# Performance work log

Hardware: AMD Instinct MI355X
Metric: run time of the kernel (lower is better)

Reference implementation:

```python
import jax, jax.numpy as jnp
import numpy as np

L, H, D, DH = 4, 16, 1024, 64   # n_layers, n_heads, d_model, head_dim
VOCAB = 32000
B, S = 2, 2048


def layer_norm(X):
    # Faithful to source: divides by variance (not std), no epsilon.
    mu = jnp.mean(X, axis=2, keepdims=True)
    var = jnp.mean((X - mu) ** 2, axis=2, keepdims=True)
    return (X - mu) / var


def setup_inputs() -> dict:
    key = jax.random.key(0)
    ks = jax.random.split(key, 12)
    s = 0.02
    X = jax.random.normal(ks[0], (B, S, D), dtype=jnp.float32)
    Wq = jax.random.normal(ks[1], (L, H, D, DH), dtype=jnp.float32) * s
    Wk = jax.random.normal(ks[2], (L, H, D, DH), dtype=jnp.float32) * s
    Wv = jax.random.normal(ks[3], (L, H, D, DH), dtype=jnp.float32) * s
    bq = jax.random.normal(ks[4], (L, H, DH), dtype=jnp.float32) * s
    bk = jax.random.normal(ks[5], (L, H, DH), dtype=jnp.float32) * s
    bv = jax.random.normal(ks[6], (L, H, DH), dtype=jnp.float32) * s
    Wffn = jax.random.normal(ks[7], (L, D, D), dtype=jnp.float32) * s
    bffn = jax.random.normal(ks[8], (L, D), dtype=jnp.float32) * s
    Wout = jax.random.normal(ks[9], (D, VOCAB), dtype=jnp.float32) * s
    bout = jax.random.normal(ks[10], (VOCAB,), dtype=jnp.float32) * s
    return {"X": X, "Wq": Wq, "Wk": Wk, "Wv": Wv, "bq": bq, "bk": bk,
            "bv": bv, "Wffn": Wffn, "bffn": bffn, "Wout": Wout, "bout": bout}


def reference(X, Wq, Wk, Wv, bq, bk, bv, Wffn, bffn, Wout, bout):
    sd = jnp.sqrt(jnp.float32(DH))
    for l in range(L):
        # All heads batched: [h, b, s, dh]
        Q = jnp.einsum('bsd,hde->hbse', X, Wq[l]) + bq[l][:, None, None, :]
        K = jnp.einsum('bsd,hde->hbse', X, Wk[l]) + bk[l][:, None, None, :]
        V = jnp.einsum('bsd,hde->hbse', X, Wv[l]) + bv[l][:, None, None, :]
        QK = jnp.einsum('hbse,hbte->hbst', Q, K) / sd
        # Faithful bug: softmax over full row, THEN tril mask (no renorm).
        A = jnp.tril(jax.nn.softmax(QK, axis=-1))
        Z = jnp.einsum('hbst,hbte->hbse', A, V)          # [h,b,s,dh]
        Z = jnp.transpose(Z, (1, 2, 0, 3)).reshape(X.shape[0], X.shape[1], D)
        X = layer_norm(X + Z)                            # note: W_o unused in source
        F = jax.nn.relu(X @ Wffn[l] + bffn[l])
        X = layer_norm(X + F)
    logits = X @ Wout + bout
    return jax.nn.softmax(logits, axis=2)[:, -1, :]
```

## Files before the change

### kernel.cpp

```cpp
#include <hip/hip_runtime.h>
#include <hip/hip_bf16.h>

#define NL 4
#define NH 16
#define DM 1024
#define DHD 64
#define NV 32000
#define NB 2
#define NS 2048
#define NM (NB * NS)

typedef __attribute__((ext_vector_type(8))) short v8s;
typedef __attribute__((ext_vector_type(4))) float v4f;

#define MFMA(a, b, c) __builtin_amdgcn_mfma_f32_16x16x32_bf16(a, b, c, 0, 0, 0)

__device__ __forceinline__ short f2bf(float x) {
    __hip_bfloat16 h = __float2bfloat16(x);
    return *reinterpret_cast<short*>(&h);
}
__device__ __forceinline__ float wave_sum(float v) {
    v += __shfl_xor(v, 32); v += __shfl_xor(v, 16); v += __shfl_xor(v, 8);
    v += __shfl_xor(v, 4);  v += __shfl_xor(v, 2);  v += __shfl_xor(v, 1);
    return v;
}
__device__ __forceinline__ float wave_max(float v) {
    v = fmaxf(v, __shfl_xor(v, 32)); v = fmaxf(v, __shfl_xor(v, 16));
    v = fmaxf(v, __shfl_xor(v, 8));  v = fmaxf(v, __shfl_xor(v, 4));
    v = fmaxf(v, __shfl_xor(v, 2));  v = fmaxf(v, __shfl_xor(v, 1));
    return v;
}

__global__ __launch_bounds__(256) void wqkv_transpose(
    const float* __restrict__ Wq, const float* __restrict__ Wk,
    const float* __restrict__ Wv, __hip_bfloat16* __restrict__ WT)
{
    __shared__ float T[64][68];
    const int t = threadIdx.x;
    const int k0 = blockIdx.x * 64;
    const int y = blockIdx.y;
    const int which = y >> 6, lh = y & 63;
    const float* W = (which == 0 ? Wq : which == 1 ? Wk : Wv)
                     + ((size_t)lh * DM + k0) * DHD;
#pragma unroll
    for (int i = 0; i < 4; ++i) {
        const int f = t + i * 256;
        const int kr = f >> 4, c = (f & 15) * 4;
        float4 w4 = *(const float4*)&W[(size_t)kr * DHD + c];
        T[kr][c + 0] = w4.x; T[kr][c + 1] = w4.y;
        T[kr][c + 2] = w4.z; T[kr][c + 3] = w4.w;
    }
    __syncthreads();
#pragma unroll
    for (int i = 0; i < 2; ++i) {
        const int f = t + i * 256;
        const int n = f >> 3, c = (f & 7) * 8;
        short tmp[8];
#pragma unroll
        for (int j = 0; j < 8; ++j) tmp[j] = f2bf(T[c + j][n]);
        *(float4*)&WT[(((size_t)y) * 64 + n) * DM + k0 + c] = *(float4*)tmp;
    }
}

__global__ __launch_bounds__(256) void wffn_transpose(
    const float* __restrict__ Wffn, __hip_bfloat16* __restrict__ WT)
{
    __shared__ float T[64][68];
    const int t = threadIdx.x;
    const int k0 = blockIdx.x * 64, n0 = blockIdx.y * 64, l = blockIdx.z;
    const float* W = Wffn + ((size_t)l * DM + k0) * DM + n0;
#pragma unroll
    for (int i = 0; i < 4; ++i) {
        const int f = t + i * 256;
        const int kr = f >> 4, c = (f & 15) * 4;
        float4 w4 = *(const float4*)&W[(size_t)kr * DM + c];
        T[kr][c + 0] = w4.x; T[kr][c + 1] = w4.y;
        T[kr][c + 2] = w4.z; T[kr][c + 3] = w4.w;
    }
    __syncthreads();
#pragma unroll
    for (int i = 0; i < 2; ++i) {
        const int f = t + i * 256;
        const int n = f >> 3, c = (f & 7) * 8;
        short tmp[8];
#pragma unroll
        for (int j = 0; j < 8; ++j) tmp[j] = f2bf(T[c + j][n]);
        *(float4*)&WT[((size_t)l * DM + n0 + n) * DM + k0 + c] = *(float4*)tmp;
    }
}

__global__ __launch_bounds__(256) void convert_x0(
    const float* __restrict__ X, __hip_bfloat16* __restrict__ Xh)
{
    const size_t i = ((size_t)blockIdx.x * 256 + threadIdx.x) * 4;
    float4 x = *(const float4*)&X[i];
    union { short s[4]; float2 f2; } hb;
    hb.s[0] = f2bf(x.x); hb.s[1] = f2bf(x.y); hb.s[2] = f2bf(x.z); hb.s[3] = f2bf(x.w);
    *(float2*)&Xh[i] = hb.f2;
}

__global__ __launch_bounds__(256, 2) void qkv_gemm(
    const __hip_bfloat16* __restrict__ Xh, const __hip_bfloat16* __restrict__ WT,
    const float* __restrict__ bq, const float* __restrict__ bk,
    const float* __restrict__ bv,
    __hip_bfloat16* __restrict__ Q, __hip_bfloat16* __restrict__ K,
    __hip_bfloat16* __restrict__ Vt, int layer)
{
    __shared__ short As[128 * 72];
    __shared__ short Bs[192 * 72];
    __shared__ short Vst[64 * 136];
    const int t = threadIdx.x;
    const int wave = t >> 6, lane = t & 63, l15 = lane & 15, quad = lane >> 4;
    const int id = blockIdx.y * 32 + blockIdx.x;
    const int x8 = id & 7, j = id >> 3;
    const int m0 = ((x8 & 3) * 8 + (j & 7)) * 128;
    const int h = (x8 >> 2) * 8 + (j >> 3);
    const int lh = layer * NH + h;
    const int arow = t >> 3, ac = (t & 7) * 8;

    v4f acc[2][12];
#pragma unroll
    for (int i = 0; i < 2; ++i)
#pragma unroll
        for (int j2 = 0; j2 < 12; ++j2) acc[i][j2] = 0.f;

    float4 ap[4], bp[6];
#pragma unroll
    for (int i = 0; i < 4; ++i)
        ap[i] = *(const float4*)&Xh[(size_t)(m0 + arow + i * 32) * DM + ac];
#pragma unroll
    for (int i = 0; i < 6; ++i) {
        const int row = arow + i * 32;
        const int which = row >> 6, dh = row & 63;
        bp[i] = *(const float4*)&WT[(((size_t)which * 64 + lh) * 64 + dh) * DM + ac];
    }

    for (int k0 = 0; k0 < DM; k0 += 64) {
        __syncthreads();
#pragma unroll
        for (int i = 0; i < 4; ++i) *(float4*)&As[(arow + i * 32) * 72 + ac] = ap[i];
#pragma unroll
        for (int i = 0; i < 6; ++i) *(float4*)&Bs[(arow + i * 32) * 72 + ac] = bp[i];
        __syncthreads();
        if (k0 + 64 < DM) {
            const int kn = k0 + 64;
#pragma unroll
            for (int i = 0; i < 4; ++i)
                ap[i] = *(const float4*)&Xh[(size_t)(m0 + arow + i * 32) * DM + kn + ac];
#pragma unroll
            for (int i = 0; i < 6; ++i) {
                const int row = arow + i * 32;
                const int which = row >> 6, dh = row & 63;
                bp[i] = *(const float4*)&WT[(((size_t)which * 64 + lh) * 64 + dh) * DM + kn + ac];
            }
        }

        v8s af[2][2];
#pragma unroll
        for (int rt = 0; rt < 2; ++rt)
#pragma unroll
            for (int kh = 0; kh < 2; ++kh)
                af[rt][kh] = *(const v8s*)&As[(wave * 32 + rt * 16 + l15) * 72 + kh * 32 + quad * 8];
#pragma unroll
        for (int ct = 0; ct < 12; ++ct) {
            v8s b0 = *(const v8s*)&Bs[(ct * 16 + l15) * 72 + quad * 8];
            v8s b1 = *(const v8s*)&Bs[(ct * 16 + l15) * 72 + 32 + quad * 8];
#pragma unroll
            for (int rt = 0; rt < 2; ++rt) {
                acc[rt][ct] = MFMA(af[rt][0], b0, acc[rt][ct]);
                acc[rt][ct] = MFMA(af[rt][1], b1, acc[rt][ct]);
            }
        }
    }

    __syncthreads();
#pragma unroll
    for (int ct = 0; ct < 4; ++ct) {
        const float bias = bq[(size_t)lh * DHD + ct * 16 + l15];
#pragma unroll
        for (int rt = 0; rt < 2; ++rt)
#pragma unroll
            for (int r = 0; r < 4; ++r) {
                const int row = wave * 32 + rt * 16 + quad * 4 + r;
                As[row * 72 + ct * 16 + l15] = f2bf(acc[rt][ct][r] + bias);
            }
    }
#pragma unroll
    for (int ct = 4; ct < 8; ++ct) {
        const float bias = bk[(size_t)lh * DHD + (ct - 4) * 16 + l15];
#pragma unroll
        for (int rt = 0; rt < 2; ++rt)
#pragma unroll
            for (int r = 0; r < 4; ++r) {
                const int row = wave * 32 + rt * 16 + quad * 4 + r;
                Bs[row * 72 + (ct - 4) * 16 + l15] = f2bf(acc[rt][ct][r] + bias);
            }
    }
#pragma unroll
    for (int ct = 8; ct < 12; ++ct) {
        const int d = (ct - 8) * 16 + l15;
        const float bias = bv[(size_t)lh * DHD + d];
#pragma unroll
        for (int rt = 0; rt < 2; ++rt)
#pragma unroll
            for (int r = 0; r < 4; ++r) {
                const int srow = wave * 32 + rt * 16 + quad * 4 + r;
                Vst[d * 136 + srow] = f2bf(acc[rt][ct][r] + bias);
            }
    }
    __syncthreads();
#pragma unroll
    for (int i = 0; i < 4; ++i) {
        const int f = t + i * 256;
        const int row = f >> 3, c = (f & 7) * 8;
        const int m = m0 + row, bb = m >> 11, s = m & (NS - 1);
        const size_t base = ((size_t)(bb * NH + h) * NS + s) * DHD + c;
        *(float4*)&Q[base] = *(const float4*)&As[row * 72 + c];
        *(float4*)&K[base] = *(const float4*)&Bs[row * 72 + c];
    }
    const int bblk = m0 >> 11;
    const int s0 = m0 & (NS - 1);
    const size_t vtb = (size_t)(bblk * NH + h) * DHD * NS;
#pragma unroll
    for (int i = 0; i < 4; ++i) {
        const int f = t + i * 256;
        const int d = f >> 4, c = (f & 15) * 8;
        *(float4*)&Vt[vtb + (size_t)d * NS + s0 + c] = *(const float4*)&Vst[d * 136 + c];
    }
}

__global__ __launch_bounds__(256, 2) void attn_kernel(
    const __hip_bfloat16* __restrict__ Q, const __hip_bfloat16* __restrict__ K,
    const __hip_bfloat16* __restrict__ Vt, float* __restrict__ Z)
{
    __shared__ short SMEM[2 * 64 * 72 + 128 * 72];
    short* Ks = SMEM;
    short* Vs = SMEM + 64 * 72;
    short* Ps = SMEM + 2 * 64 * 72;
    const int t = threadIdx.x;
    const int w = t >> 6, lane = t & 63, l15 = lane & 15, quad = lane >> 4;
    const int bh = blockIdx.x;
    const int y = blockIdx.y;
    const int bi = (y < 8) ? y : (23 - y);
    const int i0 = bi * 128;
    const int b = bh >> 4, h = bh & 15;
    const size_t qkb = (size_t)bh * NS * DHD;
    const size_t vtb = (size_t)bh * DHD * NS;
    const int arow = t >> 3, ac = (t & 7) * 8;
    const int ktd = 2 * bi;

    v8s aq[2][2];
#pragma unroll
    for (int rt = 0; rt < 2; ++rt) {
        const size_t qrow = qkb + (size_t)(i0 + w * 32 + rt * 16 + l15) * DHD + quad * 8;
        aq[rt][0] = *(const v8s*)&Q[qrow];
        aq[rt][1] = *(const v8s*)&Q[qrow + 32];
    }

    v4f o[2][4];
    float lpart[2][4];
#pragma unroll
    for (int rt = 0; rt < 2; ++rt)
#pragma unroll
        for (int i = 0; i < 4; ++i) { o[rt][i] = 0.f; lpart[rt][i] = 0.f; }

    float4 kf[2], vf[2];
#pragma unroll
    for (int i = 0; i < 2; ++i) {
        const int row = arow + i * 32;
        kf[i] = *(const float4*)&K[qkb + (size_t)row * DHD + ac];
        vf[i] = *(const float4*)&Vt[vtb + (size_t)row * NS + ac];
    }

    for (int kt = 0; kt < 32; ++kt) {
        const bool pv = (kt <= ktd + 1);
        __syncthreads();
#pragma unroll
        for (int i = 0; i < 2; ++i) {
            const int row = arow + i * 32;
            *(float4*)&Ks[row * 72 + ac] = kf[i];
            if (pv) *(float4*)&Vs[row * 72 + ac] = vf[i];
        }
        __syncthreads();
        if (kt < 31) {
            const int nt = kt + 1;
#pragma unroll
            for (int i = 0; i < 2; ++i) {
                const int row = arow + i * 32;
                kf[i] = *(const float4*)&K[qkb + (size_t)(nt * 64 + row) * DHD + ac];
                if (nt <= ktd + 1)
                    vf[i] = *(const float4*)&Vt[vtb + (size_t)row * NS + nt * 64 + ac];
            }
        }

        v4f s[2][4];
#pragma unroll
        for (int ct = 0; ct < 4; ++ct) {
            v8s b0 = *(const v8s*)&Ks[(ct * 16 + l15) * 72 + quad * 8];
            v8s b1 = *(const v8s*)&Ks[(ct * 16 + l15) * 72 + 32 + quad * 8];
#pragma unroll
            for (int rt = 0; rt < 2; ++rt) {
                v4f a = 0.f;
                a = MFMA(aq[rt][0], b0, a);
                a = MFMA(aq[rt][1], b1, a);
                s[rt][ct] = a;
            }
        }
#pragma unroll
        for (int rt = 0; rt < 2; ++rt) {
#pragma unroll
            for (int ct = 0; ct < 4; ++ct)
#pragma unroll
                for (int r = 0; r < 4; ++r)
                    s[rt][ct][r] = __expf(s[rt][ct][r] * 0.125f);
#pragma unroll
            for (int r = 0; r < 4; ++r)
                lpart[rt][r] += s[rt][0][r] + s[rt][1][r] + s[rt][2][r] + s[rt][3][r];
        }

        if (pv) {
            const int dk = kt - ktd;
#pragma unroll
            for (int rt = 0; rt < 2; ++rt)
#pragma unroll
                for (int ct = 0; ct < 4; ++ct)
#pragma unroll
                    for (int r = 0; r < 4; ++r) {
                        const int rowl = w * 32 + rt * 16 + quad * 4 + r;
                        const int col = ct * 16 + l15;
                        float pvv = s[rt][ct][r];
                        if (dk >= 0 && dk * 64 + col > rowl) pvv = 0.f;
                        Ps[rowl * 72 + col] = f2bf(pvv);
                    }
            v8s ap[2][2];
#pragma unroll
            for (int rt = 0; rt < 2; ++rt) {
                ap[rt][0] = *(const v8s*)&Ps[(w * 32 + rt * 16 + l15) * 72 + quad * 8];
                ap[rt][1] = *(const v8s*)&Ps[(w * 32 + rt * 16 + l15) * 72 + 32 + quad * 8];
            }
#pragma unroll
            for (int ct = 0; ct < 4; ++ct) {
                v8s b0 = *(const v8s*)&Vs[(ct * 16 + l15) * 72 + quad * 8];
                v8s b1 = *(const v8s*)&Vs[(ct * 16 + l15) * 72 + 32 + quad * 8];
#pragma unroll
                for (int rt = 0; rt < 2; ++rt) {
                    o[rt][ct] = MFMA(ap[rt][0], b0, o[rt][ct]);
                    o[rt][ct] = MFMA(ap[rt][1], b1, o[rt][ct]);
                }
            }
        }
    }

#pragma unroll
    for (int m = 1; m < 16; m <<= 1)
#pragma unroll
        for (int rt = 0; rt < 2; ++rt)
#pragma unroll
            for (int r = 0; r < 4; ++r)
                lpart[rt][r] += __shfl_xor(lpart[rt][r], m);

    float* Os = (float*)SMEM;
#pragma unroll
    for (int half = 0; half < 2; ++half) {
        __syncthreads();
        if ((w >> 1) == half) {
#pragma unroll
            for (int rt = 0; rt < 2; ++rt)
#pragma unroll
                for (int r = 0; r < 4; ++r) {
                    const float inv = 1.f / lpart[rt][r];
                    const int row = (w & 1) * 32 + rt * 16 + quad * 4 + r;
#pragma unroll
                    for (int ct = 0; ct < 4; ++ct)
                        Os[row * 68 + ct * 16 + l15] = o[rt][ct][r] * inv;
                }
        }
        __syncthreads();
#pragma unroll
        for (int i = 0; i < 4; ++i) {
            const int f = t + i * 256;
            const int row = f >> 4, c4 = (f & 15) * 4;
            float4 v = *(const float4*)&Os[row * 68 + c4];
            *(float4*)&Z[((size_t)b * NS + i0 + half * 64 + row) * DM + h * DHD + c4] = v;
        }
    }
}

__global__ __launch_bounds__(256, 4) void ffn_gemm(
    const __hip_bfloat16* __restrict__ Xh, const __hip_bfloat16* __restrict__ WT,
    const float* __restrict__ bffn, float* __restrict__ R, int layer)
{
    __shared__ short As[64 * 72];
    __shared__ short Bs[128 * 72];
    const int t = threadIdx.x;
    const int wave = t >> 6, lane = t & 63, l15 = lane & 15, quad = lane >> 4;
    const int m0 = blockIdx.x * 64, n0 = blockIdx.y * 128;
    const int arow = t >> 3, ac = (t & 7) * 8;

    v4f acc[8];
#pragma unroll
    for (int i = 0; i < 8; ++i) acc[i] = 0.f;

    float4 ap[2], bp[4];
#pragma unroll
    for (int i = 0; i < 2; ++i)
        ap[i] = *(const float4*)&Xh[(size_t)(m0 + arow + i * 32) * DM + ac];
#pragma unroll
    for (int i = 0; i < 4; ++i)
        bp[i] = *(const float4*)&WT[((size_t)layer * DM + n0 + arow + i * 32) * DM + ac];

    for (int k0 = 0; k0 < DM; k0 += 64) {
        __syncthreads();
#pragma unroll
        for (int i = 0; i < 2; ++i) *(float4*)&As[(arow + i * 32) * 72 + ac] = ap[i];
#pragma unroll
        for (int i = 0; i < 4; ++i) *(float4*)&Bs[(arow + i * 32) * 72 + ac] = bp[i];
        __syncthreads();
        if (k0 + 64 < DM) {
            const int kn = k0 + 64;
#pragma unroll
            for (int i = 0; i < 2; ++i)
                ap[i] = *(const float4*)&Xh[(size_t)(m0 + arow + i * 32) * DM + kn + ac];
#pragma unroll
            for (int i = 0; i < 4; ++i)
                bp[i] = *(const float4*)&WT[((size_t)layer * DM + n0 + arow + i * 32) * DM + kn + ac];
        }

        v8s af0 = *(const v8s*)&As[(wave * 16 + l15) * 72 + quad * 8];
        v8s af1 = *(const v8s*)&As[(wave * 16 + l15) * 72 + 32 + quad * 8];
#pragma unroll
        for (int ct = 0; ct < 8; ++ct) {
            v8s b0 = *(const v8s*)&Bs[(ct * 16 + l15) * 72 + quad * 8];
            v8s b1 = *(const v8s*)&Bs[(ct * 16 + l15) * 72 + 32 + quad * 8];
            acc[ct] = MFMA(af0, b0, acc[ct]);
            acc[ct] = MFMA(af1, b1, acc[ct]);
        }
    }
#pragma unroll
    for (int ct = 0; ct < 8; ++ct) {
        const int n = n0 + ct * 16 + l15;
        const float bias = bffn[(size_t)layer * DM + n];
#pragma unroll
        for (int r = 0; r < 4; ++r) {
            const int m = m0 + wave * 16 + quad * 4 + r;
            R[(size_t)m * DM + n] = fmaxf(acc[ct][r] + bias, 0.f);
        }
    }
}

__global__ __launch_bounds__(256) void add_ln(
    const float* __restrict__ Xin, const float* __restrict__ Rr,
    float* __restrict__ Xout, __hip_bfloat16* __restrict__ Xh)
{
    __shared__ float red[8];
    const int t = threadIdx.x;
    const size_t base = (size_t)blockIdx.x * DM;
    float4 x4 = *(const float4*)&Xin[base + t * 4];
    float4 r4 = *(const float4*)&Rr[base + t * 4];
    float v[4] = {x4.x + r4.x, x4.y + r4.y, x4.z + r4.z, x4.w + r4.w};
    float ssum = wave_sum(v[0] + v[1] + v[2] + v[3]);
    if ((t & 63) == 0) red[t >> 6] = ssum;
    __syncthreads();
    const float mu = (red[0] + red[1] + red[2] + red[3]) * (1.f / DM);
    float sq = 0.f;
#pragma unroll
    for (int i = 0; i < 4; ++i) { const float d = v[i] - mu; sq = fmaf(d, d, sq); }
    sq = wave_sum(sq);
    if ((t & 63) == 0) red[4 + (t >> 6)] = sq;
    __syncthreads();
    const float var = (red[4] + red[5] + red[6] + red[7]) * (1.f / DM);
    const float inv = 1.f / var;
    float4 o = {(v[0] - mu) * inv, (v[1] - mu) * inv, (v[2] - mu) * inv, (v[3] - mu) * inv};
    *(float4*)&Xout[base + t * 4] = o;
    union { short s[4]; float2 f2; } hb;
    hb.s[0] = f2bf(o.x); hb.s[1] = f2bf(o.y); hb.s[2] = f2bf(o.z); hb.s[3] = f2bf(o.w);
    *(float2*)&Xh[base + t * 4] = hb.f2;
}

__global__ __launch_bounds__(256) void last_logits2(
    const float* __restrict__ X, const float* __restrict__ Wout,
    const float* __restrict__ bout, float* __restrict__ logits)
{
    __shared__ float xs[2 * DM];
    const int t = threadIdx.x;
    for (int k = t; k < 2 * DM; k += 256) {
        const int bb = k >> 10, d = k & (DM - 1);
        xs[k] = X[((size_t)bb * NS + NS - 1) * DM + d];
    }
    __syncthreads();
    const int v = blockIdx.x * 256 + t;
    float a0 = bout[v], a1 = a0;
    for (int d = 0; d < DM; ++d) {
        const float w = Wout[(size_t)d * NV + v];
        a0 = fmaf(xs[d], w, a0);
        a1 = fmaf(xs[DM + d], w, a1);
    }
    logits[v] = a0;
    logits[NV + v] = a1;
}

__global__ __launch_bounds__(256) void final_softmax(
    const float* __restrict__ logits, float* __restrict__ out)
{
    __shared__ float red[8];
    const int b = blockIdx.x, t = threadIdx.x;
    const float* lp = logits + b * NV;
    float mx = -1e30f;
    for (int v = t; v < NV; v += 256) mx = fmaxf(mx, lp[v]);
    mx = wave_max(mx);
    if ((t & 63) == 0) red[t >> 6] = mx;
    __syncthreads();
    mx = fmaxf(fmaxf(red[0], red[1]), fmaxf(red[2], red[3]));
    float sum = 0.f;
    for (int v = t; v < NV; v += 256) sum += __expf(lp[v] - mx);
    sum = wave_sum(sum);
    if ((t & 63) == 0) red[4 + (t >> 6)] = sum;
    __syncthreads();
    sum = red[4] + red[5] + red[6] + red[7];
    const float inv = 1.f / sum;
    for (int v = t; v < NV; v += 256) out[b * NV + v] = __expf(lp[v] - mx) * inv;
}

extern "C" void kernel_launch(void* const* d_in, const int* in_sizes, int n_in,
                              void* d_out, int out_size, void* d_ws, size_t ws_size,
                              hipStream_t stream)
{
    (void)in_sizes; (void)n_in; (void)out_size; (void)ws_size;
    const float* X_in = (const float*)d_in[0];
    const float* Wq   = (const float*)d_in[1];
    const float* Wk   = (const float*)d_in[2];
    const float* Wv   = (const float*)d_in[3];
    const float* bq   = (const float*)d_in[4];
    const float* bk   = (const float*)d_in[5];
    const float* bv   = (const float*)d_in[6];
    const float* Wffn = (const float*)d_in[7];
    const float* bffn = (const float*)d_in[8];
    const float* Wout = (const float*)d_in[9];
    const float* bout = (const float*)d_in[10];
    float* out = (float*)d_out;

    const size_t NE = (size_t)NM * DM;
    char* p = (char*)d_ws;
    float* Xb = (float*)p;                    p += NE * 4;
    float* Rb = (float*)p;                    p += NE * 4;
    float* logits = (float*)p;                p += (size_t)NB * NV * 4;
    __hip_bfloat16* Xhi  = (__hip_bfloat16*)p; p += NE * 2;
    __hip_bfloat16* Qb   = (__hip_bfloat16*)p; p += NE * 2;
    __hip_bfloat16* Kb   = (__hip_bfloat16*)p; p += NE * 2;
    __hip_bfloat16* Vtb  = (__hip_bfloat16*)p; p += NE * 2;
    __hip_bfloat16* WqkvT = (__hip_bfloat16*)p; p += (size_t)3 * 64 * 64 * DM * 2;
    __hip_bfloat16* WffnT = (__hip_bfloat16*)p; p += (size_t)NL * DM * DM * 2;

    wqkv_transpose<<<dim3(16, 192), 256, 0, stream>>>(Wq, Wk, Wv, WqkvT);
    wffn_transpose<<<dim3(16, 16, NL), 256, 0, stream>>>(Wffn, WffnT);
    convert_x0<<<NM, 256, 0, stream>>>(X_in, Xhi);

    for (int l = 0; l < NL; ++l) {
        const float* Xcur = (l == 0) ? X_in : Xb;
        qkv_gemm<<<dim3(32, 16), 256, 0, stream>>>(Xhi, WqkvT, bq, bk, bv, Qb, Kb, Vtb, l);
        attn_kernel<<<dim3(32, 16), 256, 0, stream>>>(Qb, Kb, Vtb, Rb);
        add_ln<<<NM, 256, 0, stream>>>(Xcur, Rb, Xb, Xhi);
        ffn_gemm<<<dim3(64, 8), 256, 0, stream>>>(Xhi, WffnT, bffn, Rb, l);
        add_ln<<<NM, 256, 0, stream>>>(Xb, Rb, Xb, Xhi);
    }
    last_logits2<<<NV / 256, 256, 0, stream>>>(Xb, Wout, bout, logits);
    final_softmax<<<NB, 256, 0, stream>>>(logits, out);
}
```

Before: 1.399 ms.

## Software-pipeline attention loop with double-buffered K and triple-buffered V tiles

Restructures the attention inner loop so the QK^T MFMAs for tile it overlap with the softmax/PV work of tile it-1. K is double-buffered and V triple-buffered in shared memory, which cuts the loop to one barrier per iteration and prefetches two tiles ahead. It also raises wave priority around the MFMA sections. The cost is more LDS (about 64KB per block versus about 36KB), which may limit occupancy at 2 blocks per CU, and more registers for the two live score arrays.

```diff
diff --git a/kernel.cpp b/kernel.cpp
--- a/kernel.cpp
+++ b/kernel.cpp
@@ -233,10 +233,10 @@
     const __hip_bfloat16* __restrict__ Q, const __hip_bfloat16* __restrict__ K,
     const __hip_bfloat16* __restrict__ Vt, float* __restrict__ Z)
 {
-    __shared__ short SMEM[2 * 64 * 72 + 128 * 72];
-    short* Ks = SMEM;
-    short* Vs = SMEM + 64 * 72;
-    short* Ps = SMEM + 2 * 64 * 72;
+    __shared__ short SMEM[5 * 64 * 72 + 128 * 72];
+    short* Kb0 = SMEM;
+    short* Vb0 = SMEM + 2 * 64 * 72;
+    short* Ps  = SMEM + 5 * 64 * 72;
     const int t = threadIdx.x;
     const int w = t >> 6, lane = t & 63, l15 = lane & 15, quad = lane >> 4;
     const int bh = blockIdx.x;
@@ -247,14 +247,14 @@
     const size_t qkb = (size_t)bh * NS * DHD;
     const size_t vtb = (size_t)bh * DHD * NS;
     const int arow = t >> 3, ac = (t & 7) * 8;
-    const int ktd = 2 * bi;
-
-    v8s aq[2][2];
+    const int ktd = 2 * bi + 1;
+
+    v8s qf[2][2];
 #pragma unroll
     for (int rt = 0; rt < 2; ++rt) {
         const size_t qrow = qkb + (size_t)(i0 + w * 32 + rt * 16 + l15) * DHD + quad * 8;
-        aq[rt][0] = *(const v8s*)&Q[qrow];
-        aq[rt][1] = *(const v8s*)&Q[qrow + 32];
+        qf[rt][0] = *(const v8s*)&Q[qrow];
+        qf[rt][1] = *(const v8s*)&Q[qrow + 32];
     }
 
     v4f o[2][4];
@@ -271,41 +271,24 @@
         kf[i] = *(const float4*)&K[qkb + (size_t)row * DHD + ac];
         vf[i] = *(const float4*)&Vt[vtb + (size_t)row * NS + ac];
     }
-
-    for (int kt = 0; kt < 32; ++kt) {
-        const bool pv = (kt <= ktd + 1);
-        __syncthreads();
-#pragma unroll
-        for (int i = 0; i < 2; ++i) {
-            const int row = arow + i * 32;
-            *(float4*)&Ks[row * 72 + ac] = kf[i];
-            if (pv) *(float4*)&Vs[row * 72 + ac] = vf[i];
-        }
-        __syncthreads();
-        if (kt < 31) {
-            const int nt = kt + 1;
-#pragma unroll
-            for (int i = 0; i < 2; ++i) {
-                const int row = arow + i * 32;
-                kf[i] = *(const float4*)&K[qkb + (size_t)(nt * 64 + row) * DHD + ac];
-                if (nt <= ktd + 1)
-                    vf[i] = *(const float4*)&Vt[vtb + (size_t)row * NS + nt * 64 + ac];
-            }
-        }
-
-        v4f s[2][4];
-#pragma unroll
-        for (int ct = 0; ct < 4; ++ct) {
-            v8s b0 = *(const v8s*)&Ks[(ct * 16 + l15) * 72 + quad * 8];
-            v8s b1 = *(const v8s*)&Ks[(ct * 16 + l15) * 72 + 32 + quad * 8];
-#pragma unroll
-            for (int rt = 0; rt < 2; ++rt) {
-                v4f a = 0.f;
-                a = MFMA(aq[rt][0], b0, a);
-                a = MFMA(aq[rt][1], b1, a);
-                s[rt][ct] = a;
-            }
-        }
+#pragma unroll
+    for (int i = 0; i < 2; ++i) {
+        const int row = arow + i * 32;
+        *(float4*)&Kb0[row * 72 + ac] = kf[i];
+        *(float4*)&Vb0[row * 72 + ac] = vf[i];
+    }
+#pragma unroll
+    for (int i = 0; i < 2; ++i) {
+        const int row = arow + i * 32;
+        kf[i] = *(const float4*)&K[qkb + (size_t)(64 + row) * DHD + ac];
+        vf[i] = *(const float4*)&Vt[vtb + (size_t)row * NS + 64 + ac];
+    }
+    __syncthreads();
+
+    int vw = 1;
+    int vr = 2;
+
+    auto FINISH = [&](int p, v4f (&s)[2][4]) {
 #pragma unroll
         for (int rt = 0; rt < 2; ++rt) {
 #pragma unroll
@@ -317,9 +300,9 @@
             for (int r = 0; r < 4; ++r)
                 lpart[rt][r] += s[rt][0][r] + s[rt][1][r] + s[rt][2][r] + s[rt][3][r];
         }
-
-        if (pv) {
-            const int dk = kt - ktd;
+        if (p <= ktd) {
+            const int dk = p - 2 * bi;
+            const short* Vs = Vb0 + vr * 4608;
 #pragma unroll
             for (int rt = 0; rt < 2; ++rt)
 #pragma unroll
@@ -338,6 +321,7 @@
                 ap[rt][0] = *(const v8s*)&Ps[(w * 32 + rt * 16 + l15) * 72 + quad * 8];
                 ap[rt][1] = *(const v8s*)&Ps[(w * 32 + rt * 16 + l15) * 72 + 32 + quad * 8];
             }
+            __builtin_amdgcn_s_setprio(1);
 #pragma unroll
             for (int ct = 0; ct < 4; ++ct) {
                 v8s b0 = *(const v8s*)&Vs[(ct * 16 + l15) * 72 + quad * 8];
@@ -348,8 +332,62 @@
                     o[rt][ct] = MFMA(ap[rt][1], b1, o[rt][ct]);
                 }
             }
-        }
-    }
+            __builtin_amdgcn_s_setprio(0);
+        }
+    };
+
+    auto STEP = [&](int it, v4f (&scur)[2][4], v4f (&sprev)[2][4]) {
+        {
+            const short* Ks = Kb0 + (it & 1) * 4608;
+            __builtin_amdgcn_s_setprio(1);
+#pragma unroll
+            for (int ct = 0; ct < 4; ++ct) {
+                v8s b0 = *(const v8s*)&Ks[(ct * 16 + l15) * 72 + quad * 8];
+                v8s b1 = *(const v8s*)&Ks[(ct * 16 + l15) * 72 + 32 + quad * 8];
+#pragma unroll
+                for (int rt = 0; rt < 2; ++rt) {
+                    v4f a = 0.f;
+                    a = MFMA(qf[rt][0], b0, a);
+                    a = MFMA(qf[rt][1], b1, a);
+                    scur[rt][ct] = a;
+                }
+            }
+            __builtin_amdgcn_s_setprio(0);
+        }
+        if (it + 1 < 32) {
+            short* Kw = Kb0 + ((it + 1) & 1) * 4608;
+            short* Vw = Vb0 + vw * 4608;
+            const bool vneed = (it + 1 <= ktd);
+#pragma unroll
+            for (int i = 0; i < 2; ++i) {
+                const int row = arow + i * 32;
+                *(float4*)&Kw[row * 72 + ac] = kf[i];
+                if (vneed) *(float4*)&Vw[row * 72 + ac] = vf[i];
+            }
+            if (it + 2 < 32) {
+                const int T = it + 2;
+#pragma unroll
+                for (int i = 0; i < 2; ++i) {
+                    const int row = arow + i * 32;
+                    kf[i] = *(const float4*)&K[qkb + (size_t)(T * 64 + row) * DHD + ac];
+                    if (T <= ktd)
+                        vf[i] = *(const float4*)&Vt[vtb + (size_t)row * NS + T * 64 + ac];
+                }
+            }
+        }
+        if (it >= 1) FINISH(it - 1, sprev);
+        vw = (vw == 2) ? 0 : vw + 1;
+        vr = (vr == 2) ? 0 : vr + 1;
+        __syncthreads();
+    };
+
+    v4f sA[2][4], sB[2][4];
+#pragma unroll 1
+    for (int it2 = 0; it2 < 16; ++it2) {
+        STEP(2 * it2,     sA, sB);
+        STEP(2 * it2 + 1, sB, sA);
+    }
+    FINISH(31, sB);
 
 #pragma unroll
     for (int m = 1; m < 16; m <<= 1)
```

Result: no change. 1.422 ms (+1.7%).

## Split attention key range across two blocks and combine partials in add_ln

Applied to the files above, without the earlier changes.

Splits each attention block's 32 key tiles into two halves run by separate blocks, doubling the grid to 1024 blocks and raising the occupancy hint to 4. Each half writes unnormalised partial outputs and row sums, and a new add_ln_attn kernel sums the partials, normalises and applies the residual layer norm. The aim is more parallelism and better load balance for the full-row softmax, which must read every key. In exchange it adds extra global traffic for the partial buffers and a Rb aliasing onto Op0 that has to stay within size.

```diff
diff --git a/kernel.cpp b/kernel.cpp
--- a/kernel.cpp
+++ b/kernel.cpp
@@ -229,9 +229,10 @@
     }
 }
 
-__global__ __launch_bounds__(256, 2) void attn_kernel(
+__global__ __launch_bounds__(256, 4) void attn_kernel(
     const __hip_bfloat16* __restrict__ Q, const __hip_bfloat16* __restrict__ K,
-    const __hip_bfloat16* __restrict__ Vt, float* __restrict__ Z)
+    const __hip_bfloat16* __restrict__ Vt,
+    float* __restrict__ Op0, float* __restrict__ Op1, float* __restrict__ Lp)
 {
     __shared__ short SMEM[2 * 64 * 72 + 128 * 72];
     short* Ks = SMEM;
@@ -241,13 +242,17 @@
     const int w = t >> 6, lane = t & 63, l15 = lane & 15, quad = lane >> 4;
     const int bh = blockIdx.x;
     const int y = blockIdx.y;
-    const int bi = (y < 8) ? y : (23 - y);
+    const int half = y >> 4;
+    const int yt = y & 15;
+    const int bi = (yt < 8) ? yt : (23 - yt);
     const int i0 = bi * 128;
     const int b = bh >> 4, h = bh & 15;
     const size_t qkb = (size_t)bh * NS * DHD;
     const size_t vtb = (size_t)bh * DHD * NS;
     const int arow = t >> 3, ac = (t & 7) * 8;
-    const int ktd = 2 * bi;
+    const int ktd = 2 * bi + 1;
+    const int kt0 = half * 16, kt1 = kt0 + 16;
+    const bool havePV = (ktd >= kt0);
 
     v8s aq[2][2];
 #pragma unroll
@@ -268,12 +273,13 @@
 #pragma unroll
     for (int i = 0; i < 2; ++i) {
         const int row = arow + i * 32;
-        kf[i] = *(const float4*)&K[qkb + (size_t)row * DHD + ac];
-        vf[i] = *(const float4*)&Vt[vtb + (size_t)row * NS + ac];
-    }
-
-    for (int kt = 0; kt < 32; ++kt) {
-        const bool pv = (kt <= ktd + 1);
+        kf[i] = *(const float4*)&K[qkb + (size_t)(kt0 * 64 + row) * DHD + ac];
+        if (kt0 <= ktd)
+            vf[i] = *(const float4*)&Vt[vtb + (size_t)row * NS + kt0 * 64 + ac];
+    }
+
+    for (int kt = kt0; kt < kt1; ++kt) {
+        const bool pv = (kt <= ktd);
         __syncthreads();
 #pragma unroll
         for (int i = 0; i < 2; ++i) {
@@ -282,13 +288,13 @@
             if (pv) *(float4*)&Vs[row * 72 + ac] = vf[i];
         }
         __syncthreads();
-        if (kt < 31) {
+        if (kt + 1 < kt1) {
             const int nt = kt + 1;
 #pragma unroll
             for (int i = 0; i < 2; ++i) {
                 const int row = arow + i * 32;
                 kf[i] = *(const float4*)&K[qkb + (size_t)(nt * 64 + row) * DHD + ac];
-                if (nt <= ktd + 1)
+                if (nt <= ktd)
                     vf[i] = *(const float4*)&Vt[vtb + (size_t)row * NS + nt * 64 + ac];
             }
         }
@@ -319,7 +325,7 @@
         }
 
         if (pv) {
-            const int dk = kt - ktd;
+            const int dk = kt - 2 * bi;
 #pragma unroll
             for (int rt = 0; rt < 2; ++rt)
 #pragma unroll
@@ -359,20 +365,31 @@
             for (int r = 0; r < 4; ++r)
                 lpart[rt][r] += __shfl_xor(lpart[rt][r], m);
 
+    if (l15 == 0) {
+#pragma unroll
+        for (int rt = 0; rt < 2; ++rt)
+#pragma unroll
+            for (int r = 0; r < 4; ++r) {
+                const int row = i0 + w * 32 + rt * 16 + quad * 4 + r;
+                Lp[((size_t)half * 32 + bh) * NS + row] = lpart[rt][r];
+            }
+    }
+
+    if (!havePV) return;
+
     float* Os = (float*)SMEM;
 #pragma unroll
-    for (int half = 0; half < 2; ++half) {
-        __syncthreads();
-        if ((w >> 1) == half) {
+    for (int hp = 0; hp < 2; ++hp) {
+        __syncthreads();
+        if ((w >> 1) == hp) {
 #pragma unroll
             for (int rt = 0; rt < 2; ++rt)
 #pragma unroll
                 for (int r = 0; r < 4; ++r) {
-                    const float inv = 1.f / lpart[rt][r];
                     const int row = (w & 1) * 32 + rt * 16 + quad * 4 + r;
 #pragma unroll
                     for (int ct = 0; ct < 4; ++ct)
-                        Os[row * 68 + ct * 16 + l15] = o[rt][ct][r] * inv;
+                        Os[row * 68 + ct * 16 + l15] = o[rt][ct][r];
                 }
         }
         __syncthreads();
@@ -381,7 +398,11 @@
             const int f = t + i * 256;
             const int row = f >> 4, c4 = (f & 15) * 4;
             float4 v = *(const float4*)&Os[row * 68 + c4];
-            *(float4*)&Z[((size_t)b * NS + i0 + half * 64 + row) * DM + h * DHD + c4] = v;
+            const int srow = i0 + hp * 64 + row;
+            if (half == 0)
+                *(float4*)&Op0[((size_t)bh * NS + srow) * DHD + c4] = v;
+            else
+                *(float4*)&Op1[((size_t)bh * 1024 + (srow - 1024)) * DHD + c4] = v;
         }
     }
 }
@@ -446,6 +467,49 @@
             R[(size_t)m * DM + n] = fmaxf(acc[ct][r] + bias, 0.f);
         }
     }
+}
+
+__global__ __launch_bounds__(256) void add_ln_attn(
+    const float* __restrict__ Xin, const float* __restrict__ Op0,
+    const float* __restrict__ Op1, const float* __restrict__ Lp,
+    float* __restrict__ Xout, __hip_bfloat16* __restrict__ Xh)
+{
+    __shared__ float red[8];
+    const int t = threadIdx.x;
+    const int row = blockIdx.x;
+    const int b = row >> 11, s = row & (NS - 1);
+    const size_t base = (size_t)row * DM;
+    const int d = t * 4, h = d >> 6, dh = d & 63;
+    const int bh = b * NH + h;
+
+    float4 x4 = *(const float4*)&Xin[base + d];
+    float4 o4 = *(const float4*)&Op0[((size_t)bh * NS + s) * DHD + dh];
+    if (s >= 1024) {
+        float4 o1 = *(const float4*)&Op1[((size_t)bh * 1024 + (s - 1024)) * DHD + dh];
+        o4.x += o1.x; o4.y += o1.y; o4.z += o1.z; o4.w += o1.w;
+    }
+    const float l = Lp[(size_t)bh * NS + s] + Lp[((size_t)32 + bh) * NS + s];
+    const float invl = 1.f / l;
+    float v[4] = {x4.x + o4.x * invl, x4.y + o4.y * invl,
+                  x4.z + o4.z * invl, x4.w + o4.w * invl};
+
+    float ssum = wave_sum(v[0] + v[1] + v[2] + v[3]);
+    if ((t & 63) == 0) red[t >> 6] = ssum;
+    __syncthreads();
+    const float mu = (red[0] + red[1] + red[2] + red[3]) * (1.f / DM);
+    float sq = 0.f;
+#pragma unroll
+    for (int i = 0; i < 4; ++i) { const float dd = v[i] - mu; sq = fmaf(dd, dd, sq); }
+    sq = wave_sum(sq);
+    if ((t & 63) == 0) red[4 + (t >> 6)] = sq;
+    __syncthreads();
+    const float var = (red[4] + red[5] + red[6] + red[7]) * (1.f / DM);
+    const float inv = 1.f / var;
+    float4 o = {(v[0] - mu) * inv, (v[1] - mu) * inv, (v[2] - mu) * inv, (v[3] - mu) * inv};
+    *(float4*)&Xout[base + d] = o;
+    union { short sb[4]; float2 f2; } hb;
+    hb.sb[0] = f2bf(o.x); hb.sb[1] = f2bf(o.y); hb.sb[2] = f2bf(o.z); hb.sb[3] = f2bf(o.w);
+    *(float2*)&Xh[base + d] = hb.f2;
 }
 
 __global__ __launch_bounds__(256) void add_ln(
@@ -542,7 +606,10 @@
     const size_t NE = (size_t)NM * DM;
     char* p = (char*)d_ws;
     float* Xb = (float*)p;                    p += NE * 4;
-    float* Rb = (float*)p;                    p += NE * 4;
+    float* Op0 = (float*)p;                   p += (size_t)32 * NS * DHD * 4;
+    float* Rb  = Op0;
+    float* Op1 = (float*)p;                   p += (size_t)32 * 1024 * DHD * 4;
+    float* Lp  = (float*)p;                   p += (size_t)2 * 32 * NS * 4;
     float* logits = (float*)p;                p += (size_t)NB * NV * 4;
     __hip_bfloat16* Xhi  = (__hip_bfloat16*)p; p += NE * 2;
     __hip_bfloat16* Qb   = (__hip_bfloat16*)p; p += NE * 2;
@@ -558,8 +625,8 @@
     for (int l = 0; l < NL; ++l) {
         const float* Xcur = (l == 0) ? X_in : Xb;
         qkv_gemm<<<dim3(32, 16), 256, 0, stream>>>(Xhi, WqkvT, bq, bk, bv, Qb, Kb, Vtb, l);
-        attn_kernel<<<dim3(32, 16), 256, 0, stream>>>(Qb, Kb, Vtb, Rb);
-        add_ln<<<NM, 256, 0, stream>>>(Xcur, Rb, Xb, Xhi);
+        attn_kernel<<<dim3(32, 32), 256, 0, stream>>>(Qb, Kb, Vtb, Op0, Op1, Lp);
+        add_ln_attn<<<NM, 256, 0, stream>>>(Xcur, Op0, Op1, Lp, Xb, Xhi);
         ffn_gemm<<<dim3(64, 8), 256, 0, stream>>>(Xhi, WffnT, bffn, Rb, l);
         add_ln<<<NM, 256, 0, stream>>>(Xb, Rb, Xb, Xhi);
     }
```

After: 1.392 ms. About the same (-0.5%).

## Use 2x2 wave tiling in GEMMs and process two key tiles per attention sync

Applied to the files above, without the earlier changes.

The QKV and FFN GEMMs now split each block tile across waves as a 2x2 grid instead of row strips. Each wave covers a squarer sub-tile, so fewer LDS fragment loads are needed per MFMA. The attention kernel stages two 64-key K/V tiles per iteration in double-sized shared memory, which halves the number of barrier and load rounds. This raises register and LDS use per block, which may reduce occupancy.

```diff
diff --git a/kernel.cpp b/kernel.cpp
--- a/kernel.cpp
+++ b/kernel.cpp
@@ -111,6 +111,7 @@
     __shared__ short Vst[64 * 136];
     const int t = threadIdx.x;
     const int wave = t >> 6, lane = t & 63, l15 = lane & 15, quad = lane >> 4;
+    const int wm = wave >> 1, wn = wave & 1;
     const int id = blockIdx.y * 32 + blockIdx.x;
     const int x8 = id & 7, j = id >> 3;
     const int m0 = ((x8 & 3) * 8 + (j & 7)) * 128;
@@ -118,11 +119,11 @@
     const int lh = layer * NH + h;
     const int arow = t >> 3, ac = (t & 7) * 8;
 
-    v4f acc[2][12];
-#pragma unroll
-    for (int i = 0; i < 2; ++i)
-#pragma unroll
-        for (int j2 = 0; j2 < 12; ++j2) acc[i][j2] = 0.f;
+    v4f acc[4][6];
+#pragma unroll
+    for (int i = 0; i < 4; ++i)
+#pragma unroll
+        for (int j2 = 0; j2 < 6; ++j2) acc[i][j2] = 0.f;
 
     float4 ap[4], bp[6];
 #pragma unroll
@@ -155,18 +156,18 @@
             }
         }
 
-        v8s af[2][2];
-#pragma unroll
-        for (int rt = 0; rt < 2; ++rt)
+        v8s af[4][2];
+#pragma unroll
+        for (int rt = 0; rt < 4; ++rt)
 #pragma unroll
             for (int kh = 0; kh < 2; ++kh)
-                af[rt][kh] = *(const v8s*)&As[(wave * 32 + rt * 16 + l15) * 72 + kh * 32 + quad * 8];
-#pragma unroll
-        for (int ct = 0; ct < 12; ++ct) {
-            v8s b0 = *(const v8s*)&Bs[(ct * 16 + l15) * 72 + quad * 8];
-            v8s b1 = *(const v8s*)&Bs[(ct * 16 + l15) * 72 + 32 + quad * 8];
-#pragma unroll
-            for (int rt = 0; rt < 2; ++rt) {
+                af[rt][kh] = *(const v8s*)&As[(wm * 64 + rt * 16 + l15) * 72 + kh * 32 + quad * 8];
+#pragma unroll
+        for (int ct = 0; ct < 6; ++ct) {
+            v8s b0 = *(const v8s*)&Bs[(wn * 96 + ct * 16 + l15) * 72 + quad * 8];
+            v8s b1 = *(const v8s*)&Bs[(wn * 96 + ct * 16 + l15) * 72 + 32 + quad * 8];
+#pragma unroll
+            for (int rt = 0; rt < 4; ++rt) {
                 acc[rt][ct] = MFMA(af[rt][0], b0, acc[rt][ct]);
                 acc[rt][ct] = MFMA(af[rt][1], b1, acc[rt][ct]);
             }
@@ -175,37 +176,20 @@
 
     __syncthreads();
 #pragma unroll
-    for (int ct = 0; ct < 4; ++ct) {
-        const float bias = bq[(size_t)lh * DHD + ct * 16 + l15];
-#pragma unroll
-        for (int rt = 0; rt < 2; ++rt)
+    for (int ct = 0; ct < 6; ++ct) {
+        const int n = wn * 96 + ct * 16 + l15;
+        const int which = n >> 6;
+        const int dh = n & 63;
+        const float bias = (which == 0 ? bq : which == 1 ? bk : bv)[(size_t)lh * DHD + dh];
+#pragma unroll
+        for (int rt = 0; rt < 4; ++rt)
 #pragma unroll
             for (int r = 0; r < 4; ++r) {
-                const int row = wave * 32 + rt * 16 + quad * 4 + r;
-                As[row * 72 + ct * 16 + l15] = f2bf(acc[rt][ct][r] + bias);
-            }
-    }
-#pragma unroll
-    for (int ct = 4; ct < 8; ++ct) {
-        const float bias = bk[(size_t)lh * DHD + (ct - 4) * 16 + l15];
-#pragma unroll
-        for (int rt = 0; rt < 2; ++rt)
-#pragma unroll
-            for (int r = 0; r < 4; ++r) {
-                const int row = wave * 32 + rt * 16 + quad * 4 + r;
-                Bs[row * 72 + (ct - 4) * 16 + l15] = f2bf(acc[rt][ct][r] + bias);
-            }
-    }
-#pragma unroll
-    for (int ct = 8; ct < 12; ++ct) {
-        const int d = (ct - 8) * 16 + l15;
-        const float bias = bv[(size_t)lh * DHD + d];
-#pragma unroll
-        for (int rt = 0; rt < 2; ++rt)
-#pragma unroll
-            for (int r = 0; r < 4; ++r) {
-                const int srow = wave * 32 + rt * 16 + quad * 4 + r;
-                Vst[d * 136 + srow] = f2bf(acc[rt][ct][r] + bias);
+                const int row = wm * 64 + rt * 16 + quad * 4 + r;
+                const short val = f2bf(acc[rt][ct][r] + bias);
+                if (which == 0)      As[row * 72 + dh] = val;
+                else if (which == 1) Bs[row * 72 + dh] = val;
+                else                 Vst[dh * 136 + row] = val;
             }
     }
     __syncthreads();
@@ -233,10 +217,12 @@
     const __hip_bfloat16* __restrict__ Q, const __hip_bfloat16* __restrict__ K,
     const __hip_bfloat16* __restrict__ Vt, float* __restrict__ Z)
 {
-    __shared__ short SMEM[2 * 64 * 72 + 128 * 72];
-    short* Ks = SMEM;
-    short* Vs = SMEM + 64 * 72;
-    short* Ps = SMEM + 2 * 64 * 72;
+    __shared__ short SMEM[4 * 64 * 72 + 128 * 72];
+    short* Ks0 = SMEM;
+    short* Ks1 = SMEM + 4608;
+    short* Vs0 = SMEM + 2 * 4608;
+    short* Vs1 = SMEM + 3 * 4608;
+    short* Ps  = SMEM + 4 * 4608;
     const int t = threadIdx.x;
     const int w = t >> 6, lane = t & 63, l15 = lane & 15, quad = lane >> 4;
     const int bh = blockIdx.x;
@@ -247,7 +233,6 @@
     const size_t qkb = (size_t)bh * NS * DHD;
     const size_t vtb = (size_t)bh * DHD * NS;
     const int arow = t >> 3, ac = (t & 7) * 8;
-    const int ktd = 2 * bi;
 
     v8s aq[2][2];
 #pragma unroll
@@ -264,88 +249,101 @@
 #pragma unroll
         for (int i = 0; i < 4; ++i) { o[rt][i] = 0.f; lpart[rt][i] = 0.f; }
 
-    float4 kf[2], vf[2];
-#pragma unroll
-    for (int i = 0; i < 2; ++i) {
-        const int row = arow + i * 32;
-        kf[i] = *(const float4*)&K[qkb + (size_t)row * DHD + ac];
-        vf[i] = *(const float4*)&Vt[vtb + (size_t)row * NS + ac];
-    }
-
-    for (int kt = 0; kt < 32; ++kt) {
-        const bool pv = (kt <= ktd + 1);
-        __syncthreads();
+    float4 kf[4], vf[4];
+#pragma unroll
+    for (int jj = 0; jj < 2; ++jj)
 #pragma unroll
         for (int i = 0; i < 2; ++i) {
             const int row = arow + i * 32;
-            *(float4*)&Ks[row * 72 + ac] = kf[i];
-            if (pv) *(float4*)&Vs[row * 72 + ac] = vf[i];
-        }
-        __syncthreads();
-        if (kt < 31) {
-            const int nt = kt + 1;
+            kf[jj * 2 + i] = *(const float4*)&K[qkb + (size_t)(jj * 64 + row) * DHD + ac];
+            vf[jj * 2 + i] = *(const float4*)&Vt[vtb + (size_t)row * NS + jj * 64 + ac];
+        }
+
+    for (int wi = 0; wi < 16; ++wi) {
+        const bool pv = (wi <= bi);
+        __syncthreads();
+#pragma unroll
+        for (int jj = 0; jj < 2; ++jj)
 #pragma unroll
             for (int i = 0; i < 2; ++i) {
                 const int row = arow + i * 32;
-                kf[i] = *(const float4*)&K[qkb + (size_t)(nt * 64 + row) * DHD + ac];
-                if (nt <= ktd + 1)
-                    vf[i] = *(const float4*)&Vt[vtb + (size_t)row * NS + nt * 64 + ac];
-            }
-        }
-
-        v4f s[2][4];
-#pragma unroll
-        for (int ct = 0; ct < 4; ++ct) {
-            v8s b0 = *(const v8s*)&Ks[(ct * 16 + l15) * 72 + quad * 8];
-            v8s b1 = *(const v8s*)&Ks[(ct * 16 + l15) * 72 + 32 + quad * 8];
+                *(float4*)&(jj ? Ks1 : Ks0)[row * 72 + ac] = kf[jj * 2 + i];
+                if (pv) *(float4*)&(jj ? Vs1 : Vs0)[row * 72 + ac] = vf[jj * 2 + i];
+            }
+        __syncthreads();
+        if (wi < 15) {
+            const int n0t = (wi + 1) * 2;
+            const bool vneed = (wi + 1 <= bi);
+#pragma unroll
+            for (int jj = 0; jj < 2; ++jj)
+#pragma unroll
+                for (int i = 0; i < 2; ++i) {
+                    const int row = arow + i * 32;
+                    kf[jj * 2 + i] = *(const float4*)&K[qkb + (size_t)((n0t + jj) * 64 + row) * DHD + ac];
+                    if (vneed)
+                        vf[jj * 2 + i] = *(const float4*)&Vt[vtb + (size_t)row * NS + (n0t + jj) * 64 + ac];
+                }
+        }
+
+#pragma unroll
+        for (int ts = 0; ts < 2; ++ts) {
+            const short* Ks = ts ? Ks1 : Ks0;
+            const short* Vs = ts ? Vs1 : Vs0;
+
+            v4f s[2][4];
+#pragma unroll
+            for (int ct = 0; ct < 4; ++ct) {
+                v8s b0 = *(const v8s*)&Ks[(ct * 16 + l15) * 72 + quad * 8];
+                v8s b1 = *(const v8s*)&Ks[(ct * 16 + l15) * 72 + 32 + quad * 8];
+#pragma unroll
+                for (int rt = 0; rt < 2; ++rt) {
+                    v4f a = 0.f;
+                    a = MFMA(aq[rt][0], b0, a);
+                    a = MFMA(aq[rt][1], b1, a);
+                    s[rt][ct] = a;
+                }
+            }
 #pragma unroll
             for (int rt = 0; rt < 2; ++rt) {
-                v4f a = 0.f;
-                a = MFMA(aq[rt][0], b0, a);
-                a = MFMA(aq[rt][1], b1, a);
-                s[rt][ct] = a;
-            }
-        }
-#pragma unroll
-        for (int rt = 0; rt < 2; ++rt) {
-#pragma unroll
-            for (int ct = 0; ct < 4; ++ct)
+#pragma unroll
+                for (int ct = 0; ct < 4; ++ct)
+#pragma unroll
+                    for (int r = 0; r < 4; ++r)
+                        s[rt][ct][r] = __expf(s[rt][ct][r] * 0.125f);
 #pragma unroll
                 for (int r = 0; r < 4; ++r)
-                    s[rt][ct][r] = __expf(s[rt][ct][r] * 0.125f);
-#pragma unroll
-            for (int r = 0; r < 4; ++r)
-                lpart[rt][r] += s[rt][0][r] + s[rt][1][r] + s[rt][2][r] + s[rt][3][r];
-        }
-
-        if (pv) {
-            const int dk = kt - ktd;
-#pragma unroll
-            for (int rt = 0; rt < 2; ++rt)
-#pragma unroll
-                for (int ct = 0; ct < 4; ++ct)
-#pragma unroll
-                    for (int r = 0; r < 4; ++r) {
-                        const int rowl = w * 32 + rt * 16 + quad * 4 + r;
-                        const int col = ct * 16 + l15;
-                        float pvv = s[rt][ct][r];
-                        if (dk >= 0 && dk * 64 + col > rowl) pvv = 0.f;
-                        Ps[rowl * 72 + col] = f2bf(pvv);
+                    lpart[rt][r] += s[rt][0][r] + s[rt][1][r] + s[rt][2][r] + s[rt][3][r];
+            }
+
+            if (pv) {
+                const bool diag = (wi == bi);
+#pragma unroll
+                for (int rt = 0; rt < 2; ++rt)
+#pragma unroll
+                    for (int ct = 0; ct < 4; ++ct)
+#pragma unroll
+                        for (int r = 0; r < 4; ++r) {
+                            const int rowl = w * 32 + rt * 16 + quad * 4 + r;
+                            const int col = ct * 16 + l15;
+                            float pvv = s[rt][ct][r];
+                            if (diag && ts * 64 + col > rowl) pvv = 0.f;
+                            Ps[rowl * 72 + col] = f2bf(pvv);
+                        }
+                v8s ap[2][2];
+#pragma unroll
+                for (int rt = 0; rt < 2; ++rt) {
+                    ap[rt][0] = *(const v8s*)&Ps[(w * 32 + rt * 16 + l15) * 72 + quad * 8];
+                    ap[rt][1] = *(const v8s*)&Ps[(w * 32 + rt * 16 + l15) * 72 + 32 + quad * 8];
+                }
+#pragma unroll
+                for (int ct = 0; ct < 4; ++ct) {
+                    v8s b0 = *(const v8s*)&Vs[(ct * 16 + l15) * 72 + quad * 8];
+                    v8s b1 = *(const v8s*)&Vs[(ct * 16 + l15) * 72 + 32 + quad * 8];
+#pragma unroll
+                    for (int rt = 0; rt < 2; ++rt) {
+                        o[rt][ct] = MFMA(ap[rt][0], b0, o[rt][ct]);
+                        o[rt][ct] = MFMA(ap[rt][1], b1, o[rt][ct]);
                     }
-            v8s ap[2][2];
-#pragma unroll
-            for (int rt = 0; rt < 2; ++rt) {
-                ap[rt][0] = *(const v8s*)&Ps[(w * 32 + rt * 16 + l15) * 72 + quad * 8];
-                ap[rt][1] = *(const v8s*)&Ps[(w * 32 + rt * 16 + l15) * 72 + 32 + quad * 8];
-            }
-#pragma unroll
-            for (int ct = 0; ct < 4; ++ct) {
-                v8s b0 = *(const v8s*)&Vs[(ct * 16 + l15) * 72 + quad * 8];
-                v8s b1 = *(const v8s*)&Vs[(ct * 16 + l15) * 72 + 32 + quad * 8];
-#pragma unroll
-                for (int rt = 0; rt < 2; ++rt) {
-                    o[rt][ct] = MFMA(ap[rt][0], b0, o[rt][ct]);
-                    o[rt][ct] = MFMA(ap[rt][1], b1, o[rt][ct]);
                 }
             }
         }
@@ -394,12 +392,15 @@
     __shared__ short Bs[128 * 72];
     const int t = threadIdx.x;
     const int wave = t >> 6, lane = t & 63, l15 = lane & 15, quad = lane >> 4;
+    const int wm = wave >> 1, wn = wave & 1;
     const int m0 = blockIdx.x * 64, n0 = blockIdx.y * 128;
     const int arow = t >> 3, ac = (t & 7) * 8;
 
-    v4f acc[8];
-#pragma unroll
-    for (int i = 0; i < 8; ++i) acc[i] = 0.f;
+    v4f acc[2][4];
+#pragma unroll
+    for (int i = 0; i < 2; ++i)
+#pragma unroll
+        for (int j = 0; j < 4; ++j) acc[i][j] = 0.f;
 
     float4 ap[2], bp[4];
 #pragma unroll
@@ -426,25 +427,34 @@
                 bp[i] = *(const float4*)&WT[((size_t)layer * DM + n0 + arow + i * 32) * DM + kn + ac];
         }
 
-        v8s af0 = *(const v8s*)&As[(wave * 16 + l15) * 72 + quad * 8];
-        v8s af1 = *(const v8s*)&As[(wave * 16 + l15) * 72 + 32 + quad * 8];
-#pragma unroll
-        for (int ct = 0; ct < 8; ++ct) {
-            v8s b0 = *(const v8s*)&Bs[(ct * 16 + l15) * 72 + quad * 8];
-            v8s b1 = *(const v8s*)&Bs[(ct * 16 + l15) * 72 + 32 + quad * 8];
-            acc[ct] = MFMA(af0, b0, acc[ct]);
-            acc[ct] = MFMA(af1, b1, acc[ct]);
-        }
-    }
-#pragma unroll
-    for (int ct = 0; ct < 8; ++ct) {
-        const int n = n0 + ct * 16 + l15;
+        v8s af[2][2];
+#pragma unroll
+        for (int rt = 0; rt < 2; ++rt)
+#pragma unroll
+            for (int kh = 0; kh < 2; ++kh)
+                af[rt][kh] = *(const v8s*)&As[(wm * 32 + rt * 16 + l15) * 72 + kh * 32 + quad * 8];
+#pragma unroll
+        for (int ct = 0; ct < 4; ++ct) {
+            v8s b0 = *(const v8s*)&Bs[(wn * 64 + ct * 16 + l15) * 72 + quad * 8];
+            v8s b1 = *(const v8s*)&Bs[(wn * 64 + ct * 16 + l15) * 72 + 32 + quad * 8];
+#pragma unroll
+            for (int rt = 0; rt < 2; ++rt) {
+                acc[rt][ct] = MFMA(af[rt][0], b0, acc[rt][ct]);
+                acc[rt][ct] = MFMA(af[rt][1], b1, acc[rt][ct]);
+            }
+        }
+    }
+#pragma unroll
+    for (int ct = 0; ct < 4; ++ct) {
+        const int n = n0 + wn * 64 + ct * 16 + l15;
         const float bias = bffn[(size_t)layer * DM + n];
 #pragma unroll
-        for (int r = 0; r < 4; ++r) {
-            const int m = m0 + wave * 16 + quad * 4 + r;
-            R[(size_t)m * DM + n] = fmaxf(acc[ct][r] + bias, 0.f);
-        }
+        for (int rt = 0; rt < 2; ++rt)
+#pragma unroll
+            for (int r = 0; r < 4; ++r) {
+                const int m = m0 + wm * 32 + rt * 16 + quad * 4 + r;
+                R[(size_t)m * DM + n] = fmaxf(acc[rt][ct][r] + bias, 0.f);
+            }
     }
 }
 
```

Result: slower. 1.469 ms (+5.0%).
